# Optimization experiments

Hardware: AMD Instinct MI355X
Metric: run time of the kernel (lower is better)

The kernel has to match this reference:

```python
import jax, jax.numpy as jnp
import numpy as np

B, S, C, E, H, K = 32, 2048, 16, 8, 16, 2

_NLINS = [
    jax.nn.relu,                                   # relu
    jnp.tanh,                                      # tanh
    jax.nn.elu,                                    # elu
    jax.nn.silu,                                   # silu
    lambda a: a,                                   # none
    lambda a: jax.nn.gelu(a, approximate=False),   # gelu (torch default is exact erf)
    jax.nn.selu,                                   # selu
    jax.nn.softplus,                               # softplus
]


def setup_inputs() -> dict:
    key = jax.random.key(0)
    ks = jax.random.split(key, 9)
    return {
        "x": jax.random.normal(ks[0], (B, S, C, 2), dtype=jnp.float32),
        "Wm": jax.random.normal(ks[1], (E, 2 * S), dtype=jnp.float32) * 0.02,
        "bm": jax.random.normal(ks[2], (E,), dtype=jnp.float32) * 0.02,
        "Wn": jax.random.normal(ks[3], (E, 2 * S), dtype=jnp.float32) * 0.02,
        "bn": jax.random.normal(ks[4], (E,), dtype=jnp.float32) * 0.02,
        "W1": jax.random.normal(ks[5], (E, H, 3), dtype=jnp.float32) * 0.5,
        "b1": jax.random.normal(ks[6], (E, H), dtype=jnp.float32) * 0.1,
        "W2": jax.random.normal(ks[7], (E, 2, H), dtype=jnp.float32) * 0.5,
        "b2": jax.random.normal(ks[8], (E, 2), dtype=jnp.float32) * 0.1,
        "k": K,
    }


def _forward(x, Wm, bm, Wn, bn, W1, b1, W2, b2, k):
    nb, ns, nc, _ = x.shape
    ne = Wm.shape[0]
    # ---- Gate ----
    xr = jnp.swapaxes(x, 1, 2).reshape(nb * nc, 2 * ns)          # [B*C, 2S]
    g = xr @ Wm.T + bm + jax.nn.softplus(xr @ Wn.T + bn)         # [B*C, E]
    # keep_top_k: torch.kthvalue(g, n-k) = (n-k)-th smallest = sorted[:, n-k-1]
    kth = jnp.sort(g, axis=1)[:, ne - k - 1]                     # [B*C]
    g_masked = jnp.where(g > kth[:, None], g, -jnp.inf)
    gate = jax.nn.softmax(g_masked, axis=1)                      # [B*C, E]
    # ---- Experts (tiny MLPs, fixed loop over 8 distinct nonlinearities) ----
    amps = jnp.linalg.norm(x, axis=-1, keepdims=True)            # [B,S,C,1]
    feat = jnp.concatenate([x, amps], axis=-1)                   # [B,S,C,3]
    outs = []
    for e, nlin in enumerate(_NLINS):
        h = nlin(jnp.einsum('bscf,hf->bsch', feat, W1[e]) + b1[e])
        outs.append(jnp.einsum('bsch,th->bsct', h, W2[e]) + b2[e])
    eo = jnp.stack(outs)                                         # [E,B,S,C,2]
    # ---- Combine: faithful to torch row-major reshape (mixes S and C) ----
    eo_r = eo.reshape(ne, nb * nc, ns, 2)                        # [E,B*C,S,2]
    out = jnp.einsum('be,ebst->bst', gate, eo_r)                 # [B*C,S,2]
    return out.reshape(nb, nc, ns, 2).swapaxes(1, 2)             # [B,S,C,2]


def reference(x, Wm, bm, Wn, bn, W1, b1, W2, b2, k):
    return _forward(x, Wm, bm, Wn, bn, W1, b1, W2, b2, k)
```

## Files before the change

kernel.cpp:

```cpp
#include <hip/hip_runtime.h>
#include <math.h>

#define NB 32
#define NS 2048
#define NC 16
#define NE 8
#define NH 16
#define KSL 16
#define WPAD 260

__global__ __launch_bounds__(256) void gate_partial(
    const float* __restrict__ x,
    const float* __restrict__ Wm,
    const float* __restrict__ Wn,
    float* __restrict__ partial)
{
    const int b  = blockIdx.y;
    const int sl = blockIdx.x;
    const int t  = threadIdx.x;

    __shared__ float xs[128 * 32];
    __shared__ float ws[16 * WPAD];

    {
        const float* __restrict__ gx = x + b * (NS * NC * 2) + sl * 128 * 32;
#pragma unroll
        for (int rep = 0; rep < 4; ++rep) {
            const int idx = rep * 256 + t;
            *(float4*)(xs + 4 * idx) = *(const float4*)(gx + 4 * idx);
        }
    }
    {
#pragma unroll
        for (int rep = 0; rep < 4; ++rep) {
            const int idx  = rep * 256 + t;
            const int row  = idx >> 6;
            const int col4 = idx & 63;
            const float* __restrict__ gw =
                ((row < 8) ? (Wm + row * (2 * NS)) : (Wn + (row - 8) * (2 * NS)))
                + sl * 256 + col4 * 4;
            const float4 v = *(const float4*)gw;
            float* d = ws + row * WPAD + col4 * 4;
            *(float4*)d = v;
        }
    }
    __syncthreads();

    const int c = t & 15;
    const int e = t >> 4;
    const float* __restrict__ wrow = ws + e * WPAD;
    const float* __restrict__ xcol = xs + 2 * c;

    float a0 = 0.f, a1 = 0.f, a2 = 0.f, a3 = 0.f;
#pragma unroll 8
    for (int i = 0; i < 128; i += 4) {
        const float2 w0 = *(const float2*)(wrow + 2 * (i + 0));
        const float2 w1 = *(const float2*)(wrow + 2 * (i + 1));
        const float2 w2 = *(const float2*)(wrow + 2 * (i + 2));
        const float2 w3 = *(const float2*)(wrow + 2 * (i + 3));
        const float2 x0 = *(const float2*)(xcol + 32 * (i + 0));
        const float2 x1 = *(const float2*)(xcol + 32 * (i + 1));
        const float2 x2 = *(const float2*)(xcol + 32 * (i + 2));
        const float2 x3 = *(const float2*)(xcol + 32 * (i + 3));
        a0 = fmaf(x0.x, w0.x, a0); a0 = fmaf(x0.y, w0.y, a0);
        a1 = fmaf(x1.x, w1.x, a1); a1 = fmaf(x1.y, w1.y, a1);
        a2 = fmaf(x2.x, w2.x, a2); a2 = fmaf(x2.y, w2.y, a2);
        a3 = fmaf(x3.x, w3.x, a3); a3 = fmaf(x3.y, w3.y, a3);
    }
    const float acc = (a0 + a1) + (a2 + a3);
    partial[(((b * KSL) + sl) * 16 + e) * 16 + c] = acc;
}

__global__ __launch_bounds__(64) void gate_final(
    const float* __restrict__ partial,
    const float* __restrict__ bm, const float* __restrict__ bn,
    const int* __restrict__ kptr,
    float* __restrict__ gates)
{
    const int r = blockIdx.x * 64 + threadIdx.x;
    const int b = r >> 4;
    const int c = r & 15;

    float g16[16];
#pragma unroll
    for (int e = 0; e < 16; ++e) g16[e] = 0.f;
    for (int sl = 0; sl < KSL; ++sl) {
        const float* p = partial + ((b * KSL + sl) * 16) * 16 + c;
#pragma unroll
        for (int e = 0; e < 16; ++e) g16[e] += p[e * 16];
    }

    float g[NE];
#pragma unroll
    for (int e = 0; e < NE; ++e) {
        const float gn = g16[e + 8] + bn[e];
        const float sp = (gn > 20.f) ? gn : __logf(1.f + __expf(gn));
        g[e] = g16[e] + bm[e] + sp;
    }

    float s[NE];
#pragma unroll
    for (int e = 0; e < NE; ++e) s[e] = g[e];
#define CSWP(i, j) { float lo = fminf(s[i], s[j]); float hi = fmaxf(s[i], s[j]); s[i] = lo; s[j] = hi; }
    CSWP(0,1) CSWP(2,3) CSWP(4,5) CSWP(6,7)
    CSWP(0,2) CSWP(1,3) CSWP(4,6) CSWP(5,7)
    CSWP(1,2) CSWP(5,6)
    CSWP(0,4) CSWP(1,5) CSWP(2,6) CSWP(3,7)
    CSWP(2,4) CSWP(3,5)
    CSWP(1,2) CSWP(3,4) CSWP(5,6)
#undef CSWP

    const int k = *kptr;
    const float kth = s[NE - 1 - k];
    const float mx  = s[NE - 1];
    float gw[NE];
    float denom = 0.f;
#pragma unroll
    for (int e = 0; e < NE; ++e) {
        const float ex = __expf(g[e] - mx);
        const float keep = (g[e] > kth) ? ex : 0.f;
        gw[e] = keep;
        denom += keep;
    }
    const float inv = 1.f / denom;
    float4 o0 = make_float4(gw[0] * inv, gw[1] * inv, gw[2] * inv, gw[3] * inv);
    float4 o1 = make_float4(gw[4] * inv, gw[5] * inv, gw[6] * inv, gw[7] * inv);
    *(float4*)(gates + r * NE)     = o0;
    *(float4*)(gates + r * NE + 4) = o1;
}

template <int E> __device__ __forceinline__ float nlin(float v);
template <> __device__ __forceinline__ float nlin<0>(float v) { return fmaxf(v, 0.f); }
template <> __device__ __forceinline__ float nlin<1>(float v) {
    const float t = __expf(2.f * fminf(v, 15.f));
    return __fdividef(t - 1.f, t + 1.f);
}
template <> __device__ __forceinline__ float nlin<2>(float v) {
    return v > 0.f ? v : (__expf(v) - 1.f);
}
template <> __device__ __forceinline__ float nlin<3>(float v) {
    return __fdividef(v, 1.f + __expf(-v));
}
template <> __device__ __forceinline__ float nlin<4>(float v) { return v; }
template <> __device__ __forceinline__ float nlin<5>(float v) {
    const float u  = v * 0.70710678118654752f;
    const float au = fabsf(u);
    const float t  = __fdividef(1.f, fmaf(0.3275911f, au, 1.f));
    float p = fmaf(1.061405429f, t, -1.453152027f);
    p = fmaf(p, t, 1.421413741f);
    p = fmaf(p, t, -0.284496736f);
    p = fmaf(p, t, 0.254829592f);
    const float y = 1.f - p * t * __expf(-u * u);
    const float erfv = copysignf(y, u);
    return 0.5f * v * (1.f + erfv);
}
template <> __device__ __forceinline__ float nlin<6>(float v) {
    return 1.0507009873554805f * (v > 0.f ? v : 1.6732632423543772f * (__expf(v) - 1.f));
}
template <> __device__ __forceinline__ float nlin<7>(float v) {
    return (v > 20.f) ? v : __logf(1.f + __expf(v));
}

template <int E>
__device__ __forceinline__ void expert_accum2(
    const float (&xx)[2], const float (&xy)[2], const float (&am)[2], float ge,
    const float* __restrict__ W1, const float* __restrict__ b1,
    const float* __restrict__ W2, const float* __restrict__ b2,
    float (&ot0)[2], float (&ot1)[2])
{
    if (ge != 0.f) {
        float a0[2] = {0.f, 0.f}, a1[2] = {0.f, 0.f};
#pragma unroll
        for (int h = 0; h < NH; ++h) {
            const float w0  = W1[(E * NH + h) * 3 + 0];
            const float w1v = W1[(E * NH + h) * 3 + 1];
            const float w2v = W1[(E * NH + h) * 3 + 2];
            const float bb  = b1[E * NH + h];
            const float u0  = W2[E * 2 * NH + h];
            const float u1  = W2[E * 2 * NH + NH + h];
#pragma unroll
            for (int j = 0; j < 2; ++j) {
                const float pre = fmaf(w0, xx[j], fmaf(w1v, xy[j], fmaf(w2v, am[j], bb)));
                const float a = nlin<E>(pre);
                a0[j] = fmaf(u0, a, a0[j]);
                a1[j] = fmaf(u1, a, a1[j]);
            }
        }
        const float c0 = b2[E * 2 + 0];
        const float c1 = b2[E * 2 + 1];
#pragma unroll
        for (int j = 0; j < 2; ++j) {
            ot0[j] = fmaf(ge, a0[j] + c0, ot0[j]);
            ot1[j] = fmaf(ge, a1[j] + c1, ot1[j]);
        }
    }
}

__global__ __launch_bounds__(1024) void expert_kernel(
    const float* __restrict__ x,
    const float* __restrict__ W1, const float* __restrict__ b1,
    const float* __restrict__ W2, const float* __restrict__ b2,
    const float* __restrict__ gates,
    float* __restrict__ out)
{
    const int b  = blockIdx.y;
    const int s0 = blockIdx.x * 128;
    const int c    = threadIdx.x >> 6;
    const int lane = threadIdx.x & 63;

    __shared__ float lds[128 * 34];

    float g[NE];
    const float* grow = gates + (b * NC + c) * NE;
#pragma unroll
    for (int e = 0; e < NE; ++e) g[e] = grow[e];

    float xx[2], xy[2], am[2], ot0[2] = {0.f, 0.f}, ot1[2] = {0.f, 0.f};
#pragma unroll
    for (int j = 0; j < 2; ++j) {
        const int s = s0 + lane + 64 * j;
        const float2 xv = *(const float2*)(x + b * (NS * NC * 2)
                                             + (c * 128 + (s >> 4)) * (NC * 2)
                                             + (s & 15) * 2);
        xx[j] = xv.x; xy[j] = xv.y;
        am[j] = sqrtf(fmaf(xv.x, xv.x, xv.y * xv.y));
    }

    expert_accum2<0>(xx, xy, am, g[0], W1, b1, W2, b2, ot0, ot1);
    expert_accum2<1>(xx, xy, am, g[1], W1, b1, W2, b2, ot0, ot1);
    expert_accum2<2>(xx, xy, am, g[2], W1, b1, W2, b2, ot0, ot1);
    expert_accum2<3>(xx, xy, am, g[3], W1, b1, W2, b2, ot0, ot1);
    expert_accum2<4>(xx, xy, am, g[4], W1, b1, W2, b2, ot0, ot1);
    expert_accum2<5>(xx, xy, am, g[5], W1, b1, W2, b2, ot0, ot1);
    expert_accum2<6>(xx, xy, am, g[6], W1, b1, W2, b2, ot0, ot1);
    expert_accum2<7>(xx, xy, am, g[7], W1, b1, W2, b2, ot0, ot1);

#pragma unroll
    for (int j = 0; j < 2; ++j) {
        const int sl = lane + 64 * j;
        lds[sl * 34 + c * 2 + 0] = ot0[j];
        lds[sl * 34 + c * 2 + 1] = ot1[j];
    }
    __syncthreads();

#pragma unroll
    for (int j = 0; j < 2; ++j) {
        const int m  = threadIdx.x + 1024 * j;
        const int sl = m >> 4;
        const int cc = m & 15;
        float2 v = make_float2(lds[sl * 34 + cc * 2], lds[sl * 34 + cc * 2 + 1]);
        *(float2*)(out + b * (NS * NC * 2) + (s0 + sl) * (NC * 2) + cc * 2) = v;
    }
}

extern "C" void kernel_launch(void* const* d_in, const int* in_sizes, int n_in,
                              void* d_out, int out_size, void* d_ws, size_t ws_size,
                              hipStream_t stream) {
    const float* x  = (const float*)d_in[0];
    const float* Wm = (const float*)d_in[1];
    const float* bm = (const float*)d_in[2];
    const float* Wn = (const float*)d_in[3];
    const float* bn = (const float*)d_in[4];
    const float* W1 = (const float*)d_in[5];
    const float* b1 = (const float*)d_in[6];
    const float* W2 = (const float*)d_in[7];
    const float* b2 = (const float*)d_in[8];
    const int*   kp = (const int*)d_in[9];
    float* out     = (float*)d_out;
    float* gates   = (float*)d_ws;
    float* partial = (float*)d_ws + 4096;

    dim3 gp_grid(KSL, NB);
    gate_partial<<<gp_grid, 256, 0, stream>>>(x, Wm, Wn, partial);
    gate_final<<<NB * NC / 64, 64, 0, stream>>>(partial, bm, bn, kp, gates);

    dim3 grid(NS / 128, NB);
    expert_kernel<<<grid, 1024, 0, stream>>>(x, W1, b1, W2, b2, gates, out);
}
```

Before: 108.3 us.

## Split gate reduction into more K-slices and parallelize final gate reduction per row

The gate GEMV is now split into 64 S-slices instead of 16, so each block loads and reduces a smaller chunk and the grid launches four times as many blocks. gate_final now uses one 64-lane wavefront per (b,c) row: lanes split the partial-sum reduction and combine with shuffles, where before one thread serially summed all slices for its row. This targets the low parallelism of both gate kernels at the cost of a larger partial buffer and more reduction work in the final step.

```diff
diff --git a/kernel.cpp b/kernel.cpp
--- a/kernel.cpp
+++ b/kernel.cpp
@@ -6,8 +6,8 @@
 #define NC 16
 #define NE 8
 #define NH 16
-#define KSL 16
-#define WPAD 260
+#define KSL 64
+#define WPAD 68
 
 __global__ __launch_bounds__(256) void gate_partial(
     const float* __restrict__ x,
@@ -19,30 +19,20 @@
     const int sl = blockIdx.x;
     const int t  = threadIdx.x;
 
-    __shared__ float xs[128 * 32];
+    __shared__ float xs[32 * 32];
     __shared__ float ws[16 * WPAD];
 
     {
-        const float* __restrict__ gx = x + b * (NS * NC * 2) + sl * 128 * 32;
-#pragma unroll
-        for (int rep = 0; rep < 4; ++rep) {
-            const int idx = rep * 256 + t;
-            *(float4*)(xs + 4 * idx) = *(const float4*)(gx + 4 * idx);
-        }
+        const float* __restrict__ gx = x + b * (NS * NC * 2) + sl * 32 * 32;
+        *(float4*)(xs + 4 * t) = *(const float4*)(gx + 4 * t);
     }
     {
-#pragma unroll
-        for (int rep = 0; rep < 4; ++rep) {
-            const int idx  = rep * 256 + t;
-            const int row  = idx >> 6;
-            const int col4 = idx & 63;
-            const float* __restrict__ gw =
-                ((row < 8) ? (Wm + row * (2 * NS)) : (Wn + (row - 8) * (2 * NS)))
-                + sl * 256 + col4 * 4;
-            const float4 v = *(const float4*)gw;
-            float* d = ws + row * WPAD + col4 * 4;
-            *(float4*)d = v;
-        }
+        const int row  = t >> 4;
+        const int col4 = t & 15;
+        const float* __restrict__ gw =
+            ((row < 8) ? (Wm + row * (2 * NS)) : (Wn + (row - 8) * (2 * NS)))
+            + sl * 64 + col4 * 4;
+        *(float4*)(ws + row * WPAD + col4 * 4) = *(const float4*)gw;
     }
     __syncthreads();
 
@@ -52,8 +42,8 @@
     const float* __restrict__ xcol = xs + 2 * c;
 
     float a0 = 0.f, a1 = 0.f, a2 = 0.f, a3 = 0.f;
-#pragma unroll 8
-    for (int i = 0; i < 128; i += 4) {
+#pragma unroll
+    for (int i = 0; i < 32; i += 4) {
         const float2 w0 = *(const float2*)(wrow + 2 * (i + 0));
         const float2 w1 = *(const float2*)(wrow + 2 * (i + 1));
         const float2 w2 = *(const float2*)(wrow + 2 * (i + 2));
@@ -77,30 +67,36 @@
     const int* __restrict__ kptr,
     float* __restrict__ gates)
 {
-    const int r = blockIdx.x * 64 + threadIdx.x;
+    const int r = blockIdx.x;
     const int b = r >> 4;
     const int c = r & 15;
-
-    float g16[16];
-#pragma unroll
-    for (int e = 0; e < 16; ++e) g16[e] = 0.f;
-    for (int sl = 0; sl < KSL; ++sl) {
-        const float* p = partial + ((b * KSL + sl) * 16) * 16 + c;
-#pragma unroll
-        for (int e = 0; e < 16; ++e) g16[e] += p[e * 16];
-    }
-
-    float g[NE];
-#pragma unroll
-    for (int e = 0; e < NE; ++e) {
-        const float gn = g16[e + 8] + bn[e];
-        const float sp = (gn > 20.f) ? gn : __logf(1.f + __expf(gn));
-        g[e] = g16[e] + bm[e] + sp;
-    }
+    const int l = threadIdx.x;
+    const int e16    = l & 15;
+    const int sl_grp = l >> 4;
+
+    float v = 0.f;
+#pragma unroll
+    for (int j = 0; j < 16; ++j) {
+        const int sl = sl_grp * 16 + j;
+        v += partial[(((b * KSL) + sl) * 16 + e16) * 16 + c];
+    }
+    v += __shfl_xor(v, 16);
+    v += __shfl_xor(v, 32);
+
+    const int e = l & 7;
+    const float gm  = __shfl(v, e);
+    const float gnv = __shfl(v, e + 8);
+    const float gn  = gnv + bn[e];
+    const float sp  = (gn > 20.f) ? gn : __logf(1.f + __expf(gn));
+    const float g   = gm + bm[e] + sp;
+
+    float garr[NE];
+#pragma unroll
+    for (int o = 0; o < NE; ++o) garr[o] = __shfl(g, o);
 
     float s[NE];
 #pragma unroll
-    for (int e = 0; e < NE; ++e) s[e] = g[e];
+    for (int o = 0; o < NE; ++o) s[o] = garr[o];
 #define CSWP(i, j) { float lo = fminf(s[i], s[j]); float hi = fmaxf(s[i], s[j]); s[i] = lo; s[j] = hi; }
     CSWP(0,1) CSWP(2,3) CSWP(4,5) CSWP(6,7)
     CSWP(0,2) CSWP(1,3) CSWP(4,6) CSWP(5,7)
@@ -113,20 +109,15 @@
     const int k = *kptr;
     const float kth = s[NE - 1 - k];
     const float mx  = s[NE - 1];
-    float gw[NE];
     float denom = 0.f;
-#pragma unroll
-    for (int e = 0; e < NE; ++e) {
-        const float ex = __expf(g[e] - mx);
-        const float keep = (g[e] > kth) ? ex : 0.f;
-        gw[e] = keep;
-        denom += keep;
-    }
-    const float inv = 1.f / denom;
-    float4 o0 = make_float4(gw[0] * inv, gw[1] * inv, gw[2] * inv, gw[3] * inv);
-    float4 o1 = make_float4(gw[4] * inv, gw[5] * inv, gw[6] * inv, gw[7] * inv);
-    *(float4*)(gates + r * NE)     = o0;
-    *(float4*)(gates + r * NE + 4) = o1;
+    float keep_mine = 0.f;
+#pragma unroll
+    for (int o = 0; o < NE; ++o) {
+        const float ex = (garr[o] > kth) ? __expf(garr[o] - mx) : 0.f;
+        denom += ex;
+        if (o == e) keep_mine = ex;
+    }
+    if (l < NE) gates[r * NE + l] = keep_mine / denom;
 }
 
 template <int E> __device__ __forceinline__ float nlin(float v);
@@ -272,7 +263,7 @@
 
     dim3 gp_grid(KSL, NB);
     gate_partial<<<gp_grid, 256, 0, stream>>>(x, Wm, Wn, partial);
-    gate_final<<<NB * NC / 64, 64, 0, stream>>>(partial, bm, bn, kp, gates);
+    gate_final<<<NB * NC, 64, 0, stream>>>(partial, bm, bn, kp, gates);
 
     dim3 grid(NS / 128, NB);
     expert_kernel<<<grid, 1024, 0, stream>>>(x, W1, b1, W2, b2, gates, out);
```

Measured after the change: 109.8 us. About the same (+1.5%).
